# Kernel tuning notes

Hardware: AMD Instinct MI355X
Metric: run time of the kernel (lower is better)

## Reference

```python
import jax, jax.numpy as jnp
import numpy as np

N = 64000            # total nodes (64 graphs x 1000 nodes)
E = 1048576          # edges (~16 avg degree)
NB_NODES = 1000
NUM_GRAPHS = 64
F_IN, H1, H2, H3, OUT = 128, 256, 256, 128, 64


def setup_inputs() -> dict:
    key = jax.random.key(0)
    ks = jax.random.split(key, 12)
    x = jax.random.normal(ks[0], (N, F_IN), dtype=jnp.float32)
    # random edges within each graph: pick graph per edge, then local src/dst
    g = jax.random.randint(ks[1], (E,), 0, NUM_GRAPHS)
    src = g * NB_NODES + jax.random.randint(ks[2], (E,), 0, NB_NODES)
    dst = g * NB_NODES + jax.random.randint(ks[3], (E,), 0, NB_NODES)
    edge_index = jnp.stack([src, dst]).astype(jnp.int64)
    batch = (jnp.arange(N) // NB_NODES).astype(jnp.int64)  # sorted graph ids
    def glorot(k, fan_in, fan_out):
        s = jnp.sqrt(6.0 / (fan_in + fan_out))
        return jax.random.uniform(k, (fan_in, fan_out), jnp.float32, -s, s)
    return {
        "x": x, "edge_index": edge_index, "batch": batch,
        "W1": glorot(ks[4], F_IN, H1), "b1": jnp.zeros((H1,), jnp.float32),
        "W2": glorot(ks[5], H1, H2),   "b2": jnp.zeros((H2,), jnp.float32),
        "W3": glorot(ks[6], H2, H3),   "b3": jnp.zeros((H3,), jnp.float32),
        "Wfc": glorot(ks[7], H3 * NB_NODES, OUT),
        "bfc": jnp.zeros((OUT,), jnp.float32),
    }


def _gcn_norm(edge_index, n):
    # add self-loops, symmetric normalization D^-1/2 (A+I) D^-1/2
    loop = jnp.arange(n, dtype=edge_index.dtype)
    src = jnp.concatenate([edge_index[0], loop])
    dst = jnp.concatenate([edge_index[1], loop])
    deg = jax.ops.segment_sum(jnp.ones_like(src, jnp.float32), dst, num_segments=n)
    dinv = 1.0 / jnp.sqrt(deg)  # deg >= 1 thanks to self-loops
    norm = dinv[src] * dinv[dst]
    return src, dst, norm


def _gcn_layer(h, W, b, src, dst, norm, n):
    hl = h @ W                                   # [N, H]
    msg = hl[src] * norm[:, None]                # gather + scale
    agg = jax.ops.segment_sum(msg, dst, num_segments=n)  # scatter-add
    return agg + b


def reference(x, edge_index, batch, W1, b1, W2, b2, W3, b3, Wfc, bfc):
    n = x.shape[0]
    src, dst, norm = _gcn_norm(edge_index, n)
    h = jnp.tanh(_gcn_layer(x, W1, b1, src, dst, norm, n))
    h = jnp.tanh(_gcn_layer(h, W2, b2, src, dst, norm, n))
    h = jnp.tanh(_gcn_layer(h, W3, b3, src, dst, norm, n))
    # batch is sorted with equal graph sizes -> the per-graph loop/concat
    # in the original is exactly a reshape to [num_graphs, nodes*H3]
    h_concat = h.reshape(NUM_GRAPHS, NB_NODES * H3)
    return h_concat @ Wfc + bfc
```

## Files before the change

kernel.cpp:

```cpp
#include <hip/hip_runtime.h>
#include <math.h>

#define N_NODES 64000
#define N_EDGES 1048576
#define NB 1000
#define NG 64
#define NOUT 64
#define FC_SPLIT 500
#define BK_CAP 18000

typedef __attribute__((ext_vector_type(8))) short bfrag;
typedef __attribute__((ext_vector_type(4))) float f32x4;
typedef __attribute__((ext_vector_type(2))) float f32x2;

__device__ inline float bf2f(unsigned short u) {
    union { unsigned int i; float f; } x; x.i = ((unsigned int)u) << 16; return x.f;
}
__device__ inline float bflo(unsigned int u) {
    union { unsigned int i; float f; } x; x.i = u << 16; return x.f;
}
__device__ inline float bfhi(unsigned int u) {
    union { unsigned int i; float f; } x; x.i = u & 0xffff0000u; return x.f;
}
__device__ inline f32x2 upk(unsigned int u) {
    f32x2 r; r.x = bflo(u); r.y = bfhi(u); return r;
}
__device__ inline unsigned short f2bf(float f) {
    union { float f; unsigned int i; } x; x.f = f;
    return (unsigned short)((x.i + 0x7FFFu + ((x.i >> 16) & 1u)) >> 16);
}
__device__ inline float tanh_fast(float x) {
    float e = __expf(2.0f * x);
    return fmaf(-2.0f, __builtin_amdgcn_rcpf(e + 1.0f), 1.0f);
}
__device__ inline int swz32(int row, int g) { return g ^ (row & 7) ^ (g >> 3); }
__device__ inline int swz16(int row, int g) { return g ^ (row & 7) ^ (g >> 3); }

__device__ inline void gload_lds16(const unsigned short* g, unsigned short* l) {
    __builtin_amdgcn_global_load_lds(
        (const __attribute__((address_space(1))) void*)g,
        (__attribute__((address_space(3))) void*)l, 16, 0, 0);
}


__global__ __launch_bounds__(256) void k_bucket(const int* __restrict__ src,
                                                const int* __restrict__ dst,
                                                int* __restrict__ gcnt,
                                                unsigned int* __restrict__ bucket) {
    __shared__ int lcnt[64];
    __shared__ int lbase[64];
    __shared__ int lcur[64];
    int t = threadIdx.x;
    int e0 = blockIdx.x * 4096;
    if (t < 64) { lcnt[t] = 0; lcur[t] = 0; }
    __syncthreads();
    for (int i = t; i < 4096; i += 256) {
        int d = dst[e0 + i];
        int g = d / NB;
        atomicAdd(&lcnt[g], 1);
    }
    __syncthreads();
    if (t < 64) lbase[t] = atomicAdd(&gcnt[t], lcnt[t]);
    __syncthreads();
    for (int i = t; i < 4096; i += 256) {
        int d = dst[e0 + i];
        int s = src[e0 + i];
        int g = d / NB;
        int pos = atomicAdd(&lcur[g], 1);
        unsigned int packed = ((unsigned int)(d - g * NB) << 10) | (unsigned int)(s - g * NB);
        bucket[(size_t)g * BK_CAP + lbase[g] + pos] = packed;
    }
}

__global__ __launch_bounds__(1024) void k_build(const int* __restrict__ gcnt,
                                                const unsigned int* __restrict__ bucket,
                                                int* __restrict__ rowptr,
                                                int* __restrict__ rowend,
                                                float* __restrict__ dinv,
                                                unsigned short* __restrict__ colp) {
    __shared__ int ind[1024];
    __shared__ int tmp[1024];
    int t = threadIdx.x;
    int g = blockIdx.x;
    int cnt = gcnt[g];
    size_t base = (size_t)g * BK_CAP;
    ind[t] = 0;
    __syncthreads();
    for (int i = t; i < cnt; i += 1024) {
        unsigned int p = bucket[base + i];
        atomicAdd(&ind[p >> 10], 1);
    }
    __syncthreads();
    int deg = ind[t];
    if (t < NB) dinv[g * NB + t] = rsqrtf((float)(deg + 1));
    tmp[t] = deg;
    __syncthreads();
    for (int off = 1; off < 1024; off <<= 1) {
        int o = (t >= off) ? tmp[t - off] : 0;
        __syncthreads();
        tmp[t] += o;
        __syncthreads();
    }
    int excl = tmp[t] - deg;
    if (t < NB) {
        rowptr[g * NB + t] = (int)base + excl;
        rowend[g * NB + t] = (int)base + excl + deg;
    }
    ind[t] = excl;
    __syncthreads();
    for (int i = t; i < cnt; i += 1024) {
        unsigned int p = bucket[base + i];
        int dl = p >> 10;
        int pos = atomicAdd(&ind[dl], 1);
        colp[base + pos] = (unsigned short)(p & 1023u);
    }
}


__global__ void k_cast_scale(const float* __restrict__ in, const float* __restrict__ dinv,
                             unsigned short* __restrict__ out) {
    int i = (blockIdx.x * blockDim.x + threadIdx.x) * 4;
    float d = dinv[i >> 7];
    float4 v = *(const float4*)(in + i);
    union { unsigned short s[4]; uint2 u; } o;
    o.s[0] = f2bf(v.x * d); o.s[1] = f2bf(v.y * d);
    o.s[2] = f2bf(v.z * d); o.s[3] = f2bf(v.w * d);
    *(uint2*)(out + i) = o.u;
}

__global__ void k_wt(const float* __restrict__ W, unsigned short* __restrict__ Wt,
                     int K, int N) {
    int i = blockIdx.x * 256 + threadIdx.x;
    if (i < K * N) {
        int n = i / K, k = i % K;
        Wt[i] = f2bf(W[k * N + n]);
    }
}


template <int H, bool TANH>
__global__ void k_agg(const unsigned short* __restrict__ hs, unsigned short* __restrict__ op,
                      const int* __restrict__ rowptr, const int* __restrict__ rowend,
                      const unsigned short* __restrict__ col,
                      const float* __restrict__ dinv, const float* __restrict__ bias) {
    constexpr int VEC = H / 64;
    int lane = threadIdx.x & 63;
    int b = blockIdx.x;
    int c = b & 7;
    int j = b >> 3;
    int g = c + 8 * (j / 250);
    int chunk = j % 250;
    int v = g * NB + chunk * 4 + (threadIdx.x >> 6);
    const unsigned short* gb = hs + (size_t)g * NB * H;
    f32x2 a0, a1;
    {
        const unsigned short* r = hs + (size_t)v * H + lane * VEC;
        if (VEC == 2) {
            a0 = upk(*(const unsigned int*)r);
        } else {
            uint2 u = *(const uint2*)r;
            a0 = upk(u.x); a1 = upk(u.y);
        }
    }
    int beg = rowptr[v], end = rowend[v];
    for (int e0 = beg; e0 < end; e0 += 64) {
        int me = e0 + lane;
        int s = (me < end) ? (int)col[me] : 0;
        int cnt = min(64, end - e0);
        int i = 0;
        for (; i + 8 <= cnt; i += 8) {
            int sx[8];
#pragma unroll
            for (int q = 0; q < 8; ++q) sx[q] = __builtin_amdgcn_readlane(s, i + q);
            if (VEC == 2) {
                unsigned int u[8];
#pragma unroll
                for (int q = 0; q < 8; ++q)
                    u[q] = *(const unsigned int*)(gb + (size_t)sx[q] * H + lane * 2);
#pragma unroll
                for (int q = 0; q < 8; ++q) a0 += upk(u[q]);
            } else {
                uint2 u[8];
#pragma unroll
                for (int q = 0; q < 8; ++q)
                    u[q] = *(const uint2*)(gb + (size_t)sx[q] * H + lane * 4);
#pragma unroll
                for (int q = 0; q < 8; ++q) { a0 += upk(u[q].x); a1 += upk(u[q].y); }
            }
        }
        for (; i + 4 <= cnt; i += 4) {
            int sx[4];
#pragma unroll
            for (int q = 0; q < 4; ++q) sx[q] = __builtin_amdgcn_readlane(s, i + q);
            if (VEC == 2) {
                unsigned int u[4];
#pragma unroll
                for (int q = 0; q < 4; ++q)
                    u[q] = *(const unsigned int*)(gb + (size_t)sx[q] * H + lane * 2);
#pragma unroll
                for (int q = 0; q < 4; ++q) a0 += upk(u[q]);
            } else {
                uint2 u[4];
#pragma unroll
                for (int q = 0; q < 4; ++q)
                    u[q] = *(const uint2*)(gb + (size_t)sx[q] * H + lane * 4);
#pragma unroll
                for (int q = 0; q < 4; ++q) { a0 += upk(u[q].x); a1 += upk(u[q].y); }
            }
        }
        for (; i < cnt; ++i) {
            int ss = __builtin_amdgcn_readlane(s, i);
            if (VEC == 2) {
                a0 += upk(*(const unsigned int*)(gb + (size_t)ss * H + lane * 2));
            } else {
                uint2 u = *(const uint2*)(gb + (size_t)ss * H + lane * 4);
                a0 += upk(u.x); a1 += upk(u.y);
            }
        }
    }
    float dv = dinv[v];
    float acc[4];
    acc[0] = a0.x; acc[1] = a0.y;
    if (VEC == 4) { acc[2] = a1.x; acc[3] = a1.y; }
    if (TANH) {
#pragma unroll
        for (int q = 0; q < VEC; ++q) acc[q] = tanh_fast(acc[q] * dv + bias[lane * VEC + q]);
    } else {
#pragma unroll
        for (int q = 0; q < VEC; ++q) acc[q] *= dv;
    }
    unsigned short* o = op + (size_t)v * H + lane * VEC;
    if (VEC == 2) {
        union { unsigned short s[2]; unsigned int u; } pk;
        pk.s[0] = f2bf(acc[0]); pk.s[1] = f2bf(acc[1]);
        *(unsigned int*)o = pk.u;
    } else {
        union { unsigned short s[4]; uint2 u; } pk;
        pk.s[0] = f2bf(acc[0]); pk.s[1] = f2bf(acc[1]);
        pk.s[2] = f2bf(acc[2]); pk.s[3] = f2bf(acc[3]);
        *(uint2*)o = pk.u;
    }
}


__global__ __launch_bounds__(256, 2) void k_gemm1(const unsigned short* __restrict__ A,
                                                  const unsigned short* __restrict__ W1t,
                                                  const float* __restrict__ b1,
                                                  const float* __restrict__ dinv,
                                                  unsigned short* __restrict__ C) {
    constexpr int K = 128, N = 256;
    __shared__ unsigned short at[64 * 128];
    int t = threadIdx.x;
    int w = t >> 6, l = t & 63;
    int lm = l & 15, lq = l >> 4;
    int n0 = w * 64;
    int row0 = lq * 4;
    int m0 = blockIdx.x * 64;

    {
        const unsigned short* Ab = A + (size_t)m0 * K;
#pragma unroll
        for (int q = 0; q < 4; ++q) {
            int rbase = w * 16 + q * 4;
            int row = rbase + (l >> 4);
            int g = swz16(row, l & 15);
            gload_lds16(Ab + (size_t)row * K + g * 8, &at[rbase * K]);
        }
    }
    bfrag B1[16];
    {
        const unsigned short* Bb = W1t + (size_t)(n0 + lm) * K + lq * 8;
#pragma unroll
        for (int j = 0; j < 4; ++j)
#pragma unroll
            for (int it = 0; it < 4; ++it)
                B1[j * 4 + it] = *(const bfrag*)(Bb + (size_t)j * 16 * K + it * 32);
    }
    float bj[4];
#pragma unroll
    for (int j = 0; j < 4; ++j) bj[j] = b1[n0 + j * 16 + lm];

    asm volatile("s_waitcnt vmcnt(0)\n\ts_barrier" ::: "memory");

    f32x4 acc[4][4] = {};
#pragma unroll
    for (int it = 0; it < 4; ++it) {
        bfrag af[4];
        int gidx = it * 4 + lq;
#pragma unroll
        for (int i = 0; i < 4; ++i) {
            int row = i * 16 + lm;
            af[i] = *(const bfrag*)&at[row * K + swz16(row, gidx) * 8];
        }
#pragma unroll
        for (int i = 0; i < 4; ++i)
#pragma unroll
            for (int j = 0; j < 4; ++j)
                acc[i][j] = __builtin_amdgcn_mfma_f32_16x16x32_bf16(af[i], B1[j * 4 + it], acc[i][j], 0, 0, 0);
    }
    float drow[4][4];
#pragma unroll
    for (int i = 0; i < 4; ++i)
#pragma unroll
        for (int r = 0; r < 4; ++r) drow[i][r] = dinv[m0 + i * 16 + row0 + r];
#pragma unroll
    for (int i = 0; i < 4; ++i)
#pragma unroll
        for (int j = 0; j < 4; ++j)
#pragma unroll
            for (int r = 0; r < 4; ++r) {
                float v = tanh_fast(acc[i][j][r] + bj[j]) * drow[i][r];
                C[(size_t)(m0 + i * 16 + row0 + r) * N + n0 + j * 16 + lm] = f2bf(v);
            }
}


__global__ __launch_bounds__(256, 2) void k_gemm23(const unsigned short* __restrict__ A,
                                                   const unsigned short* __restrict__ W2t,
                                                   const float* __restrict__ b2,
                                                   const unsigned short* __restrict__ W3t,
                                                   const float* __restrict__ dinv,
                                                   unsigned short* __restrict__ C) {
    constexpr int K = 256, N3 = 128;
    __shared__ unsigned short at[64 * 256];
    int t = threadIdx.x;
    int w = t >> 6, l = t & 63;
    int lm = l & 15, lq = l >> 4;
    int n0 = w * 64;
    int row0 = lq * 4;
    int m0 = blockIdx.x * 64;
    int n3 = w * 32;
    const unsigned short* B3b = W3t + (size_t)(n3 + lm) * K + lq * 8;

    {
        const unsigned short* Ab = A + (size_t)m0 * K;
#pragma unroll
        for (int q = 0; q < 8; ++q) {
            int rbase = w * 16 + q * 2;
            int row = rbase + (l >> 5);
            int g = swz32(row, l & 31);
            gload_lds16(Ab + (size_t)row * K + g * 8, &at[rbase * K]);
        }
    }
    bfrag B1[32];
    {
        const unsigned short* Bb = W2t + (size_t)(n0 + lm) * K + lq * 8;
#pragma unroll
        for (int j = 0; j < 4; ++j)
#pragma unroll
            for (int it = 0; it < 8; ++it)
                B1[j * 8 + it] = *(const bfrag*)(Bb + (size_t)j * 16 * K + it * 32);
    }
    bfrag bfb[4][2];
#pragma unroll
    for (int p = 0; p < 2; ++p)
#pragma unroll
        for (int j = 0; j < 2; ++j)
            bfb[p][j] = *(const bfrag*)(B3b + (size_t)j * 16 * K + p * 32);
    float bj[4];
#pragma unroll
    for (int j = 0; j < 4; ++j) bj[j] = b2[n0 + j * 16 + lm];

    asm volatile("s_waitcnt vmcnt(0)\n\ts_barrier" ::: "memory");

    f32x4 acc[4][4] = {};
#pragma unroll
    for (int it = 0; it < 8; ++it) {
        bfrag af[4];
        int gidx = it * 4 + lq;
#pragma unroll
        for (int i = 0; i < 4; ++i) {
            int row = i * 16 + lm;
            af[i] = *(const bfrag*)&at[row * 256 + swz32(row, gidx) * 8];
        }
#pragma unroll
        for (int i = 0; i < 4; ++i)
#pragma unroll
            for (int j = 0; j < 4; ++j)
                acc[i][j] = __builtin_amdgcn_mfma_f32_16x16x32_bf16(af[i], B1[j * 8 + it], acc[i][j], 0, 0, 0);
    }
    asm volatile("s_waitcnt lgkmcnt(0)\n\ts_barrier" ::: "memory");
#pragma unroll
    for (int i = 0; i < 4; ++i)
#pragma unroll
        for (int j = 0; j < 4; ++j) {
            int colb = n0 + j * 16 + lm;
            int gidx = colb >> 3, off = colb & 7;
#pragma unroll
            for (int r = 0; r < 4; ++r) {
                int row = i * 16 + row0 + r;
                at[row * 256 + swz32(row, gidx) * 8 + off] =
                    f2bf(tanh_fast(acc[i][j][r] + bj[j]));
            }
        }
    asm volatile("s_waitcnt lgkmcnt(0)\n\ts_barrier" ::: "memory");
    {
        f32x4 acc2[4][2] = {};
#pragma unroll
        for (int it = 0; it < 8; ++it) {
            if (it + 2 < 8) {
#pragma unroll
                for (int j = 0; j < 2; ++j)
                    bfb[(it + 2) & 3][j] = *(const bfrag*)(B3b + (size_t)j * 16 * K + (it + 2) * 32);
            }
            bfrag af[4];
            int gidx = it * 4 + lq;
#pragma unroll
            for (int i = 0; i < 4; ++i) {
                int row = i * 16 + lm;
                af[i] = *(const bfrag*)&at[row * 256 + swz32(row, gidx) * 8];
            }
#pragma unroll
            for (int i = 0; i < 4; ++i)
#pragma unroll
                for (int j = 0; j < 2; ++j)
                    acc2[i][j] = __builtin_amdgcn_mfma_f32_16x16x32_bf16(af[i], bfb[it & 3][j], acc2[i][j], 0, 0, 0);
        }
        float drow[4][4];
#pragma unroll
        for (int i = 0; i < 4; ++i)
#pragma unroll
            for (int r = 0; r < 4; ++r) drow[i][r] = dinv[m0 + i * 16 + row0 + r];
#pragma unroll
        for (int i = 0; i < 4; ++i)
#pragma unroll
            for (int j = 0; j < 2; ++j)
#pragma unroll
                for (int r = 0; r < 4; ++r)
                    C[(size_t)(m0 + i * 16 + row0 + r) * N3 + n3 + j * 16 + lm] =
                        f2bf(acc2[i][j][r] * drow[i][r]);
    }
}


__global__ void k_fc(const unsigned short* __restrict__ A, const float* __restrict__ B,
                     float* __restrict__ part) {
    __shared__ float As[16][68];
    __shared__ float Bs[16][68];
    const int KROW = NB * 128;
    int t = threadIdx.x;
    int tx = t & 15, ty = t >> 4;
    int k0b = blockIdx.x * 256;
    float acc[4][4] = {};
    for (int k0 = k0b; k0 < k0b + 256; k0 += 16) {
        int arow = t >> 2, ak = (t & 3) << 2;
        uint2 ua = *(const uint2*)(A + (size_t)arow * KROW + k0 + ak);
        As[ak + 0][arow] = bflo(ua.x);
        As[ak + 1][arow] = bfhi(ua.x);
        As[ak + 2][arow] = bflo(ua.y);
        As[ak + 3][arow] = bfhi(ua.y);
        int bk = t >> 4, bn4 = (t & 15) << 2;
        *(float4*)&Bs[bk][bn4] = *(const float4*)(B + (size_t)(k0 + bk) * NOUT + bn4);
        __syncthreads();
#pragma unroll
        for (int kk = 0; kk < 16; ++kk) {
            float4 a = *(const float4*)&As[kk][ty << 2];
            float4 b = *(const float4*)&Bs[kk][tx << 2];
            acc[0][0] += a.x * b.x; acc[0][1] += a.x * b.y; acc[0][2] += a.x * b.z; acc[0][3] += a.x * b.w;
            acc[1][0] += a.y * b.x; acc[1][1] += a.y * b.y; acc[1][2] += a.y * b.z; acc[1][3] += a.y * b.w;
            acc[2][0] += a.z * b.x; acc[2][1] += a.z * b.y; acc[2][2] += a.z * b.z; acc[2][3] += a.z * b.w;
            acc[3][0] += a.w * b.x; acc[3][1] += a.w * b.y; acc[3][2] += a.w * b.z; acc[3][3] += a.w * b.w;
        }
        __syncthreads();
    }
    float* po = part + (size_t)blockIdx.x * (NG * NOUT);
#pragma unroll
    for (int i = 0; i < 4; ++i) {
        float4 r;
        r.x = acc[i][0]; r.y = acc[i][1]; r.z = acc[i][2]; r.w = acc[i][3];
        *(float4*)&po[((ty << 2) + i) * NOUT + (tx << 2)] = r;
    }
}

__global__ void k_fc_reduce(const float* __restrict__ part, const float* __restrict__ bfc,
                            float* __restrict__ out) {
    int i = blockIdx.x * blockDim.x + threadIdx.x;
    float s = bfc[i & 63];
    for (int b = 0; b < FC_SPLIT; ++b) s += part[(size_t)b * (NG * NOUT) + i];
    out[i] = s;
}


static inline size_t align256(size_t x) { return (x + 255) & ~(size_t)255; }

extern "C" void kernel_launch(void* const* d_in, const int* in_sizes, int n_in,
                              void* d_out, int out_size, void* d_ws, size_t ws_size,
                              hipStream_t stream) {
    const float* x   = (const float*)d_in[0];
    const int*   ei  = (const int*)d_in[1];
    const int*   src = ei;
    const int*   dst = ei + N_EDGES;
    const float* W1  = (const float*)d_in[3];
    const float* b1  = (const float*)d_in[4];
    const float* W2  = (const float*)d_in[5];
    const float* b2  = (const float*)d_in[6];
    const float* W3  = (const float*)d_in[7];
    const float* b3  = (const float*)d_in[8];
    const float* Wfc = (const float*)d_in[9];
    const float* bfc = (const float*)d_in[10];
    float* out = (float*)d_out;

    char* w = (char*)d_ws;
    unsigned short* P0 = (unsigned short*)w; w += align256((size_t)N_NODES * 256 * 2);
    unsigned short* P1 = (unsigned short*)w; w += align256((size_t)N_NODES * 256 * 2);
    unsigned short* P2 = (unsigned short*)w; w += align256((size_t)N_NODES * 256 * 2);
    int* rowptr = (int*)w;      w += align256((size_t)N_NODES * 4);
    int* rowend = (int*)w;      w += align256((size_t)N_NODES * 4);
    float* dinv = (float*)w;    w += align256((size_t)N_NODES * 4);
    int* gcnt = (int*)w;        w += align256((size_t)NG * 4);
    unsigned int* bucket = (unsigned int*)w; w += align256((size_t)NG * BK_CAP * 4);
    unsigned short* colp = (unsigned short*)w; w += align256((size_t)NG * BK_CAP * 2);
    float* fcpart = (float*)w;  w += align256((size_t)FC_SPLIT * NG * NOUT * 4);
    unsigned short* W1t = (unsigned short*)w; w += align256((size_t)128 * 256 * 2);
    unsigned short* W2t = (unsigned short*)w; w += align256((size_t)256 * 256 * 2);
    unsigned short* W3t = (unsigned short*)w; w += align256((size_t)256 * 128 * 2);

    hipMemsetAsync(gcnt, 0, (size_t)NG * 4, stream);
    k_bucket<<<N_EDGES / 4096, 256, 0, stream>>>(src, dst, gcnt, bucket);
    k_build<<<NG, 1024, 0, stream>>>(gcnt, bucket, rowptr, rowend, dinv, colp);

    k_cast_scale<<<(N_NODES * 128 / 4) / 256, 256, 0, stream>>>(x, dinv, P0);
    k_wt<<<(128 * 256 + 255) / 256, 256, 0, stream>>>(W1, W1t, 128, 256);
    k_wt<<<(256 * 256 + 255) / 256, 256, 0, stream>>>(W2, W2t, 256, 256);
    k_wt<<<(256 * 128 + 255) / 256, 256, 0, stream>>>(W3, W3t, 256, 128);

    k_agg<128, false><<<N_NODES / 4, 256, 0, stream>>>(P0, P1, rowptr, rowend, colp, dinv, nullptr);
    k_gemm1<<<N_NODES / 64, 256, 0, stream>>>(P1, W1t, b1, dinv, P2);

    k_agg<256, false><<<N_NODES / 4, 256, 0, stream>>>(P2, P0, rowptr, rowend, colp, dinv, nullptr);
    k_gemm23<<<N_NODES / 64, 256, 0, stream>>>(P0, W2t, b2, W3t, dinv, P1);

    k_agg<128, true><<<N_NODES / 4, 256, 0, stream>>>(P1, P0, rowptr, rowend, colp, dinv, b3);

    k_fc<<<FC_SPLIT, 256, 0, stream>>>(P0, Wfc, fcpart);
    k_fc_reduce<<<NG * NOUT / 256, 256, 0, stream>>>(fcpart, bfc, out);
}
```

Measured before the change: 342.4 us.

## Stage per-graph feature slices in LDS for neighbor aggregation

Replaces the global-memory gather aggregation with a kernel that loads each graph's 1000-node, 64-column feature slice into shared memory (padded to 33 words per row to avoid bank conflicts), then gathers neighbor rows from LDS. Each block of 1024 threads handles one graph and one 64-column chunk; the two half-waves split the edge list and are combined with a shuffle. This is meant to turn scattered global/L2 gathers into LDS reads. The trade-off is a much smaller grid (256 blocks of 1024 threads), about 132KB of LDS per block which limits occupancy, and redundant reads of the edge list per column chunk.

```diff
diff --git a/kernel.cpp b/kernel.cpp
--- a/kernel.cpp
+++ b/kernel.cpp
@@ -13,9 +13,6 @@
 typedef __attribute__((ext_vector_type(4))) float f32x4;
 typedef __attribute__((ext_vector_type(2))) float f32x2;
 
-__device__ inline float bf2f(unsigned short u) {
-    union { unsigned int i; float f; } x; x.i = ((unsigned int)u) << 16; return x.f;
-}
 __device__ inline float bflo(unsigned int u) {
     union { unsigned int i; float f; } x; x.i = u << 16; return x.f;
 }
@@ -139,106 +136,94 @@
 
 
 template <int H, bool TANH>
-__global__ void k_agg(const unsigned short* __restrict__ hs, unsigned short* __restrict__ op,
-                      const int* __restrict__ rowptr, const int* __restrict__ rowend,
-                      const unsigned short* __restrict__ col,
-                      const float* __restrict__ dinv, const float* __restrict__ bias) {
-    constexpr int VEC = H / 64;
-    int lane = threadIdx.x & 63;
+__global__ __launch_bounds__(1024) void k_agg_lds(const unsigned short* __restrict__ hs,
+                                                  unsigned short* __restrict__ op,
+                                                  const int* __restrict__ rowptr,
+                                                  const int* __restrict__ rowend,
+                                                  const unsigned short* __restrict__ col,
+                                                  const float* __restrict__ dinv,
+                                                  const float* __restrict__ bias) {
+    constexpr int NCH = H / 64;
+    constexpr int NHALF = 4 / NCH;
+    constexpr int NDST = NB / NHALF;
+    __shared__ unsigned int L[NB * 33];
+    int t = threadIdx.x;
+    int w = t >> 6, l = t & 63;
+    int l31 = l & 31, hf = l >> 5;
     int b = blockIdx.x;
-    int c = b & 7;
-    int j = b >> 3;
-    int g = c + 8 * (j / 250);
-    int chunk = j % 250;
-    int v = g * NB + chunk * 4 + (threadIdx.x >> 6);
-    const unsigned short* gb = hs + (size_t)g * NB * H;
-    f32x2 a0, a1;
+    int g = b >> 2;
+    int sub = b & 3;
+    int ch, hh;
+    if constexpr (NCH == 4) { ch = sub; hh = 0; }
+    else                    { ch = sub >> 1; hh = sub & 1; }
+    int c0 = ch * 64;
+    const unsigned short* gb = hs + (size_t)g * NB * H + c0;
+
     {
-        const unsigned short* r = hs + (size_t)v * H + lane * VEC;
-        if (VEC == 2) {
-            a0 = upk(*(const unsigned int*)r);
+        int rr = t >> 3, cc = t & 7;
+        for (int r0 = rr; r0 < NB; r0 += 128) {
+            uint4 v = *(const uint4*)(gb + (size_t)r0 * H + cc * 8);
+            unsigned int* p = &L[r0 * 33 + cc * 4];
+            p[0] = v.x; p[1] = v.y; p[2] = v.z; p[3] = v.w;
+        }
+    }
+    __syncthreads();
+
+    float bx = 0.f, by = 0.f;
+    if (TANH) { bx = bias[c0 + 2 * l31]; by = bias[c0 + 2 * l31 + 1]; }
+
+    int dst0 = hh * NDST;
+    for (int d = dst0 + w; d < dst0 + NDST; d += 16) {
+        int v = g * NB + d;
+        int beg = rowptr[v], end = rowend[v];
+        f32x2 acc = {0.f, 0.f};
+        if (!hf) acc = upk(L[d * 33 + l31]);
+        for (int e0 = beg; e0 < end; e0 += 64) {
+            int me = e0 + l;
+            int s = (me < end) ? (int)col[me] : 0;
+            int cnt = min(64, end - e0);
+            int i = 0;
+            for (; i + 8 <= cnt; i += 8) {
+                int r[4];
+#pragma unroll
+                for (int q = 0; q < 4; ++q) {
+                    int sA = __builtin_amdgcn_readlane(s, i + 2 * q);
+                    int sB = __builtin_amdgcn_readlane(s, i + 2 * q + 1);
+                    r[q] = hf ? sB : sA;
+                }
+                unsigned int u[4];
+#pragma unroll
+                for (int q = 0; q < 4; ++q) u[q] = L[r[q] * 33 + l31];
+#pragma unroll
+                for (int q = 0; q < 4; ++q) acc += upk(u[q]);
+            }
+            for (; i + 2 <= cnt; i += 2) {
+                int sA = __builtin_amdgcn_readlane(s, i);
+                int sB = __builtin_amdgcn_readlane(s, i + 1);
+                int row = hf ? sB : sA;
+                acc += upk(L[row * 33 + l31]);
+            }
+            if (i < cnt) {
+                int sA = __builtin_amdgcn_readlane(s, i);
+                if (!hf) acc += upk(L[sA * 33 + l31]);
+            }
+        }
+        acc.x += __shfl_xor(acc.x, 32);
+        acc.y += __shfl_xor(acc.y, 32);
+        float dv = dinv[v];
+        float rx, ry;
+        if (TANH) {
+            rx = tanh_fast(acc.x * dv + bx);
+            ry = tanh_fast(acc.y * dv + by);
         } else {
-            uint2 u = *(const uint2*)r;
-            a0 = upk(u.x); a1 = upk(u.y);
-        }
-    }
-    int beg = rowptr[v], end = rowend[v];
-    for (int e0 = beg; e0 < end; e0 += 64) {
-        int me = e0 + lane;
-        int s = (me < end) ? (int)col[me] : 0;
-        int cnt = min(64, end - e0);
-        int i = 0;
-        for (; i + 8 <= cnt; i += 8) {
-            int sx[8];
-#pragma unroll
-            for (int q = 0; q < 8; ++q) sx[q] = __builtin_amdgcn_readlane(s, i + q);
-            if (VEC == 2) {
-                unsigned int u[8];
-#pragma unroll
-                for (int q = 0; q < 8; ++q)
-                    u[q] = *(const unsigned int*)(gb + (size_t)sx[q] * H + lane * 2);
-#pragma unroll
-                for (int q = 0; q < 8; ++q) a0 += upk(u[q]);
-            } else {
-                uint2 u[8];
-#pragma unroll
-                for (int q = 0; q < 8; ++q)
-                    u[q] = *(const uint2*)(gb + (size_t)sx[q] * H + lane * 4);
-#pragma unroll
-                for (int q = 0; q < 8; ++q) { a0 += upk(u[q].x); a1 += upk(u[q].y); }
-            }
-        }
-        for (; i + 4 <= cnt; i += 4) {
-            int sx[4];
-#pragma unroll
-            for (int q = 0; q < 4; ++q) sx[q] = __builtin_amdgcn_readlane(s, i + q);
-            if (VEC == 2) {
-                unsigned int u[4];
-#pragma unroll
-                for (int q = 0; q < 4; ++q)
-                    u[q] = *(const unsigned int*)(gb + (size_t)sx[q] * H + lane * 2);
-#pragma unroll
-                for (int q = 0; q < 4; ++q) a0 += upk(u[q]);
-            } else {
-                uint2 u[4];
-#pragma unroll
-                for (int q = 0; q < 4; ++q)
-                    u[q] = *(const uint2*)(gb + (size_t)sx[q] * H + lane * 4);
-#pragma unroll
-                for (int q = 0; q < 4; ++q) { a0 += upk(u[q].x); a1 += upk(u[q].y); }
-            }
-        }
-        for (; i < cnt; ++i) {
-            int ss = __builtin_amdgcn_readlane(s, i);
-            if (VEC == 2) {
-                a0 += upk(*(const unsigned int*)(gb + (size_t)ss * H + lane * 2));
-            } else {
-                uint2 u = *(const uint2*)(gb + (size_t)ss * H + lane * 4);
-                a0 += upk(u.x); a1 += upk(u.y);
-            }
-        }
-    }
-    float dv = dinv[v];
-    float acc[4];
-    acc[0] = a0.x; acc[1] = a0.y;
-    if (VEC == 4) { acc[2] = a1.x; acc[3] = a1.y; }
-    if (TANH) {
-#pragma unroll
-        for (int q = 0; q < VEC; ++q) acc[q] = tanh_fast(acc[q] * dv + bias[lane * VEC + q]);
-    } else {
-#pragma unroll
-        for (int q = 0; q < VEC; ++q) acc[q] *= dv;
-    }
-    unsigned short* o = op + (size_t)v * H + lane * VEC;
-    if (VEC == 2) {
-        union { unsigned short s[2]; unsigned int u; } pk;
-        pk.s[0] = f2bf(acc[0]); pk.s[1] = f2bf(acc[1]);
-        *(unsigned int*)o = pk.u;
-    } else {
-        union { unsigned short s[4]; uint2 u; } pk;
-        pk.s[0] = f2bf(acc[0]); pk.s[1] = f2bf(acc[1]);
-        pk.s[2] = f2bf(acc[2]); pk.s[3] = f2bf(acc[3]);
-        *(uint2*)o = pk.u;
+            rx = acc.x * dv;
+            ry = acc.y * dv;
+        }
+        if (!hf) {
+            union { unsigned short s2[2]; unsigned int u; } pk;
+            pk.s2[0] = f2bf(rx); pk.s2[1] = f2bf(ry);
+            *(unsigned int*)(op + (size_t)v * H + c0 + 2 * l31) = pk.u;
+        }
     }
 }
 
@@ -524,13 +509,13 @@
     k_wt<<<(256 * 256 + 255) / 256, 256, 0, stream>>>(W2, W2t, 256, 256);
     k_wt<<<(256 * 128 + 255) / 256, 256, 0, stream>>>(W3, W3t, 256, 128);
 
-    k_agg<128, false><<<N_NODES / 4, 256, 0, stream>>>(P0, P1, rowptr, rowend, colp, dinv, nullptr);
+    k_agg_lds<128, false><<<256, 1024, 0, stream>>>(P0, P1, rowptr, rowend, colp, dinv, nullptr);
     k_gemm1<<<N_NODES / 64, 256, 0, stream>>>(P1, W1t, b1, dinv, P2);
 
-    k_agg<256, false><<<N_NODES / 4, 256, 0, stream>>>(P2, P0, rowptr, rowend, colp, dinv, nullptr);
+    k_agg_lds<256, false><<<256, 1024, 0, stream>>>(P2, P0, rowptr, rowend, colp, dinv, nullptr);
     k_gemm23<<<N_NODES / 64, 256, 0, stream>>>(P0, W2t, b2, W3t, dinv, P1);
 
-    k_agg<128, true><<<N_NODES / 4, 256, 0, stream>>>(P1, P0, rowptr, rowend, colp, dinv, b3);
+    k_agg_lds<128, true><<<256, 1024, 0, stream>>>(P1, P0, rowptr, rowend, colp, dinv, b3);
 
     k_fc<<<FC_SPLIT, 256, 0, stream>>>(P0, Wfc, fcpart);
     k_fc_reduce<<<NG * NOUT / 256, 256, 0, stream>>>(fcpart, bfc, out);
```

After: 445.5 us. +30.1%, slower.
